# Performance work log

Hardware: AMD Instinct MI355X
Metric: run time of the kernel (lower is better)

Reference implementation:

```python
import jax, jax.numpy as jnp
import numpy as np

B, T, D_IN, D_H, D_OUT = 32, 2048, 1024, 1024, 1024

def setup_inputs() -> dict:
    key = jax.random.key(0)
    k1, k2, k3, k4, k5 = jax.random.split(key, 5)
    s = jax.random.normal(k1, (B, D_IN), dtype=jnp.float32)
    h = jax.random.normal(k2, (B, T, D_H), dtype=jnp.float32)
    # params (original uses np.random.random, i.e. uniform [0,1); scale kept modest)
    W_a = jax.random.uniform(k3, (D_IN, D_OUT), dtype=jnp.float32)
    U_a = jax.random.uniform(k4, (D_H, D_OUT), dtype=jnp.float32)
    v_a = jax.random.uniform(k5, (D_OUT,), dtype=jnp.float32)
    return {"s": s, "h": h, "W_a": W_a, "U_a": U_a, "v_a": v_a}

def reference(s, h, W_a, U_a, v_a):
    # Bahdanau additive attention:
    # e_bt = v_a . tanh(s W_a + h_t U_a);  a = softmax_t(e);  c_b = sum_t a_bt h_bt
    u_a_h = jnp.einsum('bth,ho->bto', h, U_a)            # [B,T,O]
    w_a_s = jnp.einsum('bi,io->bo', s, W_a)[:, None, :]  # [B,1,O]
    e = jnp.einsum('bto,o->bt', jnp.tanh(w_a_s + u_a_h), v_a)  # [B,T]
    a = jax.nn.softmax(e, axis=-1)                       # [B,T]
    c = jnp.einsum('bt,bth->bh', a, h)                   # [B,H]
    return c
```

## Files before the change

kernel.cpp:

```cpp
#include <hip/hip_runtime.h>
#include <hip/hip_bf16.h>
#include <stdint.h>

#define Bb 32
#define Tt 2048
#define Dd 1024

typedef float    f32x4 __attribute__((ext_vector_type(4)));
typedef _Float16 f16x8 __attribute__((ext_vector_type(8)));
typedef uint32_t u32;

#define WS_E     131072
#define WS_A     393216
#define WS_CP    655360
#define WS_UT    4849664

__device__ __forceinline__ void gll16(const void* g, const void* lds) {
  __builtin_amdgcn_global_load_lds(
      (const __attribute__((address_space(1))) u32*)(uintptr_t)g,
      (__attribute__((address_space(3))) u32*)(uint32_t)(uintptr_t)lds,
      16, 0, 0);
}

__global__ __launch_bounds__(256) void k_ws(const float* __restrict__ s,
                                            const float* __restrict__ W,
                                            float* __restrict__ w2_ws) {
  const int b = blockIdx.x >> 2;
  const int o = (blockIdx.x & 3) * 256 + threadIdx.x;
  __shared__ float s_sh[Dd];
#pragma unroll
  for (int j = 0; j < 4; ++j)
    s_sh[threadIdx.x + 256 * j] = s[b * Dd + threadIdx.x + 256 * j];
  __syncthreads();
  float acc = 0.f;
#pragma unroll 8
  for (int i = 0; i < Dd; ++i) acc += s_sh[i] * W[(size_t)i * Dd + o];
  w2_ws[b * Dd + o] = 2.f * acc;
}

__global__ __launch_bounds__(256) void k_ut(const float* __restrict__ U,
                                            uint8_t* __restrict__ U_ts) {
  const int i0 = (blockIdx.x >> 4) * 64;
  const int o0 = (blockIdx.x & 15) * 64;
  __shared__ float tile[64][65];
  const int tx = threadIdx.x & 63;
  const int ty = threadIdx.x >> 6;
#pragma unroll
  for (int jj = 0; jj < 16; ++jj)
    tile[tx][ty + 4 * jj] = U[(size_t)(i0 + ty + 4 * jj) * Dd + o0 + tx];
  __syncthreads();
#pragma unroll
  for (int it = 0; it < 2; ++it) {
    const int g = it * 256 + threadIdx.x;
    const int o_loc = g & 63;
    const int kg = g >> 6;
    const int o = o0 + o_loc;
    const int k = i0 + kg * 8;
    f16x8 r;
#pragma unroll
    for (int m = 0; m < 8; ++m) r[m] = (_Float16)tile[o_loc][kg * 8 + m];
    const int c    = (o >> 5) * 4 + (k >> 8);
    const int kk   = (k >> 5) & 7;
    const int half = (o >> 4) & 1;
    const int ln   = ((k >> 3) & 3) * 16 + (o & 15);
    *(f16x8*)(U_ts + (size_t)c * 16384 + kk * 2048 + half * 1024 + ln * 16) = r;
  }
}

__global__ __launch_bounds__(256, 2) void k_e(const float* __restrict__ h,
                                              const uint8_t* __restrict__ U_ts,
                                              const float* __restrict__ w2_ws,
                                              const float* __restrict__ v_a,
                                              float* __restrict__ e_ws) {
  const int b    = blockIdx.x >> 5;
  const int t0   = (blockIdx.x & 31) << 6;
  const int lane = threadIdx.x & 63;
  const int wv   = threadIdx.x >> 6;
  const int kh   = wv & 1;
  const int th   = wv >> 1;

  __shared__ __align__(16) uint8_t ubuf[3][16384];
  __shared__ __align__(16) float   exch[2048];
  __shared__ float w_sh[Dd];
  __shared__ float v_sh[Dd];

#pragma unroll
  for (int j = 0; j < 4; ++j) {
    const int o = threadIdx.x + 256 * j;
    w_sh[o] = w2_ws[b * Dd + o];
    v_sh[o] = v_a[o];
  }

  f16x8 hreg[32];
  {
    const int tcol = t0 + th * 32 + (lane & 15);
    const int kgrp = (lane >> 4) * 8;
    const float* hb0 = h + ((size_t)b * Tt + tcol) * Dd;
    const float* hb1 = hb0 + (size_t)16 * Dd;
#pragma unroll
    for (int ss = 0; ss < 16; ++ss) {
      const int kbase = (ss >> 2) * 256 + kh * 128 + (ss & 3) * 32 + kgrp;
      f32x4 p0 = *(const f32x4*)(hb0 + kbase);
      f32x4 p1 = *(const f32x4*)(hb0 + kbase + 4);
      f16x8 r;
      r[0] = (_Float16)p0[0]; r[1] = (_Float16)p0[1];
      r[2] = (_Float16)p0[2]; r[3] = (_Float16)p0[3];
      r[4] = (_Float16)p1[0]; r[5] = (_Float16)p1[1];
      r[6] = (_Float16)p1[2]; r[7] = (_Float16)p1[3];
      hreg[ss * 2] = r;
      p0 = *(const f32x4*)(hb1 + kbase);
      p1 = *(const f32x4*)(hb1 + kbase + 4);
      r[0] = (_Float16)p0[0]; r[1] = (_Float16)p0[1];
      r[2] = (_Float16)p0[2]; r[3] = (_Float16)p0[3];
      r[4] = (_Float16)p1[0]; r[5] = (_Float16)p1[1];
      r[6] = (_Float16)p1[2]; r[7] = (_Float16)p1[3];
      hreg[ss * 2 + 1] = r;
    }
  }

  asm volatile("s_waitcnt vmcnt(0) lgkmcnt(0)" ::: "memory");

  auto stage = [&](int c, int buf) {
    const uint8_t* src = U_ts + (size_t)c * 16384 + (size_t)(wv * 4) * 1024 + (size_t)lane * 16;
#pragma unroll
    for (int q = 0; q < 4; ++q)
      gll16(src + q * 1024, &ubuf[buf][(wv * 4 + q) * 1024]);
  };

  stage(0, 0);
  stage(1, 1);

  float ep0 = 0.f, ep1 = 0.f;
  const int obl = kh * 16 + ((lane >> 4) << 2);
  int cur = 0;

  for (int ot = 0; ot < 32; ++ot) {
    f32x4 accA0 = {0.f,0.f,0.f,0.f}, accA1 = {0.f,0.f,0.f,0.f};
    f32x4 accB0 = {0.f,0.f,0.f,0.f}, accB1 = {0.f,0.f,0.f,0.f};
#pragma unroll
    for (int kc = 0; kc < 4; ++kc) {
      const int c = ot * 4 + kc;
      asm volatile("s_waitcnt vmcnt(4)" ::: "memory");
      __builtin_amdgcn_sched_barrier(0);
      __builtin_amdgcn_s_barrier();
      __builtin_amdgcn_sched_barrier(0);
      const int nxt = cur >= 1 ? cur - 1 : cur + 2;
      stage((c + 2) & 127, nxt);
      const uint8_t* ub = &ubuf[cur][0] + kh * 8192 + lane * 16;
      __builtin_amdgcn_s_setprio(1);
#pragma unroll
      for (int kkl = 0; kkl < 4; ++kkl) {
        const f16x8 a0 = *(const f16x8*)(ub + kkl * 2048);
        const f16x8 a1 = *(const f16x8*)(ub + kkl * 2048 + 1024);
        const f16x8 b0 = hreg[(kc * 4 + kkl) * 2];
        const f16x8 b1 = hreg[(kc * 4 + kkl) * 2 + 1];
        accA0 = __builtin_amdgcn_mfma_f32_16x16x32_f16(a0, b0, accA0, 0, 0, 0);
        accA1 = __builtin_amdgcn_mfma_f32_16x16x32_f16(a0, b1, accA1, 0, 0, 0);
        accB0 = __builtin_amdgcn_mfma_f32_16x16x32_f16(a1, b0, accB0, 0, 0, 0);
        accB1 = __builtin_amdgcn_mfma_f32_16x16x32_f16(a1, b1, accB1, 0, 0, 0);
      }
      __builtin_amdgcn_s_setprio(0);
      cur = cur == 2 ? 0 : cur + 1;
    }
    {
      float* snd = exch + wv * 512 + lane * 4;
      if (kh == 0) { *(f32x4*)snd = accB0; *(f32x4*)(snd + 256) = accB1; }
      else         { *(f32x4*)snd = accA0; *(f32x4*)(snd + 256) = accA1; }
    }
    asm volatile("s_waitcnt lgkmcnt(0)" ::: "memory");
    __builtin_amdgcn_sched_barrier(0);
    __builtin_amdgcn_s_barrier();
    __builtin_amdgcn_sched_barrier(0);
    {
      const float* rcv = exch + (wv ^ 1) * 512 + lane * 4;
      const f32x4 q0 = *(const f32x4*)rcv;
      const f32x4 q1 = *(const f32x4*)(rcv + 256);
      f32x4 x0, x1;
      if (kh == 0) { x0 = accA0 + q0; x1 = accA1 + q1; }
      else         { x0 = accB0 + q0; x1 = accB1 + q1; }
      const int ob = (ot << 5) + obl;
#pragma unroll
      for (int r = 0; r < 4; ++r) {
        const float wr = w_sh[ob + r];
        const float vr = v_sh[ob + r];
        const float e0 = __expf(__builtin_fmaf(x0[r], 2.f, wr));
        const float e1 = __expf(__builtin_fmaf(x1[r], 2.f, wr));
        ep0 += vr * (1.f - 2.f / (e0 + 1.f));
        ep1 += vr * (1.f - 2.f / (e1 + 1.f));
      }
    }
  }

  ep0 += __shfl_xor(ep0, 16, 64); ep0 += __shfl_xor(ep0, 32, 64);
  ep1 += __shfl_xor(ep1, 16, 64); ep1 += __shfl_xor(ep1, 32, 64);
  __syncthreads();
  if (kh == 1 && lane < 16) {
    exch[th * 32 + lane]      = ep0;
    exch[th * 32 + 16 + lane] = ep1;
  }
  __syncthreads();
  if (kh == 0 && lane < 16) {
    e_ws[b * Tt + t0 + th * 32 + lane]      = ep0 + exch[th * 32 + lane];
    e_ws[b * Tt + t0 + th * 32 + 16 + lane] = ep1 + exch[th * 32 + 16 + lane];
  }
}

__global__ __launch_bounds__(256) void k_sm(const float* __restrict__ e_ws,
                                            float* __restrict__ a_ws) {
  const int b = blockIdx.x;
  const int lane = threadIdx.x & 63;
  const int wv = threadIdx.x >> 6;
  __shared__ float red[8];
  float ev[8];
  float m = -1e30f;
#pragma unroll
  for (int j = 0; j < 8; ++j) {
    ev[j] = e_ws[b * Tt + threadIdx.x + 256 * j];
    m = fmaxf(m, ev[j]);
  }
#pragma unroll
  for (int sft = 1; sft < 64; sft <<= 1) m = fmaxf(m, __shfl_xor(m, sft, 64));
  if (lane == 0) red[wv] = m;
  __syncthreads();
  m = fmaxf(fmaxf(red[0], red[1]), fmaxf(red[2], red[3]));
  float sum = 0.f;
#pragma unroll
  for (int j = 0; j < 8; ++j) { ev[j] = __expf(ev[j] - m); sum += ev[j]; }
#pragma unroll
  for (int sft = 1; sft < 64; sft <<= 1) sum += __shfl_xor(sum, sft, 64);
  if (lane == 0) red[4 + wv] = sum;
  __syncthreads();
  const float inv = 1.f / (red[4] + red[5] + red[6] + red[7]);
#pragma unroll
  for (int j = 0; j < 8; ++j) a_ws[b * Tt + threadIdx.x + 256 * j] = ev[j] * inv;
}

__global__ __launch_bounds__(256) void k_c1(const float* __restrict__ h,
                                            const float* __restrict__ a_ws,
                                            float* __restrict__ cpart) {
  const int b  = blockIdx.x >> 5;
  const int tc = blockIdx.x & 31;
  const int t0 = tc << 6;
  __shared__ float a_sh[64];
  if (threadIdx.x < 64) a_sh[threadIdx.x] = a_ws[b * Tt + t0 + threadIdx.x];
  __syncthreads();
  f32x4 acc = {0.f, 0.f, 0.f, 0.f};
  const float* hb = h + ((size_t)b * Tt + t0) * Dd + threadIdx.x * 4;
#pragma unroll 4
  for (int t = 0; t < 64; ++t) {
    const f32x4 hv = *(const f32x4*)(hb + (size_t)t * Dd);
    acc += a_sh[t] * hv;
  }
  *(f32x4*)(cpart + ((size_t)(tc * 32 + b) << 10) + threadIdx.x * 4) = acc;
}

__global__ __launch_bounds__(256) void k_c2(const float* __restrict__ cpart,
                                            float* __restrict__ out) {
  const int gid = blockIdx.x * 256 + threadIdx.x;
  const int b = gid >> 10;
  const int d = gid & 1023;
  float sv = 0.f;
#pragma unroll
  for (int tc = 0; tc < 32; ++tc) sv += cpart[((size_t)(tc * 32 + b) << 10) + d];
  out[gid] = sv;
}

extern "C" void kernel_launch(void* const* d_in, const int* in_sizes, int n_in,
                              void* d_out, int out_size, void* d_ws, size_t ws_size,
                              hipStream_t stream) {
  (void)in_sizes; (void)n_in; (void)out_size; (void)ws_size;
  const float* s  = (const float*)d_in[0];
  const float* h  = (const float*)d_in[1];
  const float* W  = (const float*)d_in[2];
  const float* U  = (const float*)d_in[3];
  const float* v  = (const float*)d_in[4];
  uint8_t* ws = (uint8_t*)d_ws;
  float*   w2_ws = (float*)ws;
  float*   e_ws  = (float*)(ws + WS_E);
  float*   a_ws  = (float*)(ws + WS_A);
  float*   cpart = (float*)(ws + WS_CP);
  uint8_t* U_ts  = ws + WS_UT;

  k_ws<<<128, 256, 0, stream>>>(s, W, w2_ws);
  k_ut<<<256, 256, 0, stream>>>(U, U_ts);
  k_e <<<1024, 256, 0, stream>>>(h, U_ts, w2_ws, v, e_ws);
  k_sm<<<Bb, 256, 0, stream>>>(e_ws, a_ws);
  k_c1<<<1024, 256, 0, stream>>>(h, a_ws, cpart);
  k_c2<<<128, 256, 0, stream>>>(cpart, (float*)d_out);
}
```

Before: 301.2 us.

## Split k_e reduction across 8 waves with two-stage cross-wave exchange

The scoring kernel now runs 512 threads per block. Each wave holds a quarter of the K dimension of h in registers (16 fragments instead of 32) and partial tiles are reduced across waves through two LDS exchange rounds. U staging drops from triple to double buffering with a full vmcnt(0) wait before each chunk. The aim is to cut VGPR pressure and raise occupancy and latency hiding. The cost is an extra barrier and exchange round per output tile and less prefetch depth.

Result: slower. 310.0 us (+2.9%).

```diff
diff --git a/kernel.cpp b/kernel.cpp
--- a/kernel.cpp
+++ b/kernel.cpp
@@ -67,142 +67,143 @@
   }
 }
 
-__global__ __launch_bounds__(256, 2) void k_e(const float* __restrict__ h,
+__global__ __launch_bounds__(512, 4) void k_e(const float* __restrict__ h,
                                               const uint8_t* __restrict__ U_ts,
                                               const float* __restrict__ w2_ws,
                                               const float* __restrict__ v_a,
                                               float* __restrict__ e_ws) {
   const int b    = blockIdx.x >> 5;
   const int t0   = (blockIdx.x & 31) << 6;
-  const int lane = threadIdx.x & 63;
-  const int wv   = threadIdx.x >> 6;
-  const int kh   = wv & 1;
-  const int th   = wv >> 1;
-
-  __shared__ __align__(16) uint8_t ubuf[3][16384];
-  __shared__ __align__(16) float   exch[2048];
+  const int tid  = threadIdx.x;
+  const int lane = tid & 63;
+  const int w    = tid >> 6;
+  const int th   = w >> 2;
+  const int kq   = w & 3;
+
+  __shared__ __align__(16) uint8_t ubuf[2][16384];
+  __shared__ __align__(16) float   exchA[4096];
+  __shared__ __align__(16) float   exchB[2048];
   __shared__ float w_sh[Dd];
   __shared__ float v_sh[Dd];
 
 #pragma unroll
-  for (int j = 0; j < 4; ++j) {
-    const int o = threadIdx.x + 256 * j;
+  for (int j = 0; j < 2; ++j) {
+    const int o = tid + 512 * j;
     w_sh[o] = w2_ws[b * Dd + o];
     v_sh[o] = v_a[o];
   }
 
-  f16x8 hreg[32];
+  f16x8 hreg[16];
   {
-    const int tcol = t0 + th * 32 + (lane & 15);
-    const int kgrp = (lane >> 4) * 8;
-    const float* hb0 = h + ((size_t)b * Tt + tcol) * Dd;
-    const float* hb1 = hb0 + (size_t)16 * Dd;
-#pragma unroll
-    for (int ss = 0; ss < 16; ++ss) {
-      const int kbase = (ss >> 2) * 256 + kh * 128 + (ss & 3) * 32 + kgrp;
-      f32x4 p0 = *(const f32x4*)(hb0 + kbase);
-      f32x4 p1 = *(const f32x4*)(hb0 + kbase + 4);
-      f16x8 r;
-      r[0] = (_Float16)p0[0]; r[1] = (_Float16)p0[1];
-      r[2] = (_Float16)p0[2]; r[3] = (_Float16)p0[3];
-      r[4] = (_Float16)p1[0]; r[5] = (_Float16)p1[1];
-      r[6] = (_Float16)p1[2]; r[7] = (_Float16)p1[3];
-      hreg[ss * 2] = r;
-      p0 = *(const f32x4*)(hb1 + kbase);
-      p1 = *(const f32x4*)(hb1 + kbase + 4);
-      r[0] = (_Float16)p0[0]; r[1] = (_Float16)p0[1];
-      r[2] = (_Float16)p0[2]; r[3] = (_Float16)p0[3];
-      r[4] = (_Float16)p1[0]; r[5] = (_Float16)p1[1];
-      r[6] = (_Float16)p1[2]; r[7] = (_Float16)p1[3];
-      hreg[ss * 2 + 1] = r;
-    }
-  }
-
-  asm volatile("s_waitcnt vmcnt(0) lgkmcnt(0)" ::: "memory");
+    const int lr = lane & 15, lg = (lane >> 4) * 8;
+#pragma unroll
+    for (int kc = 0; kc < 4; ++kc)
+#pragma unroll
+      for (int kkl = 0; kkl < 2; ++kkl)
+#pragma unroll
+        for (int tc = 0; tc < 2; ++tc) {
+          const int trow = t0 + th * 32 + tc * 16 + lr;
+          const int k = kc * 256 + kq * 64 + kkl * 32 + lg;
+          const float* p = h + ((size_t)b * Tt + trow) * Dd + k;
+          const f32x4 p0 = *(const f32x4*)p;
+          const f32x4 p1 = *(const f32x4*)(p + 4);
+          f16x8 r;
+          r[0] = (_Float16)p0[0]; r[1] = (_Float16)p0[1];
+          r[2] = (_Float16)p0[2]; r[3] = (_Float16)p0[3];
+          r[4] = (_Float16)p1[0]; r[5] = (_Float16)p1[1];
+          r[6] = (_Float16)p1[2]; r[7] = (_Float16)p1[3];
+          hreg[(kc * 2 + kkl) * 2 + tc] = r;
+        }
+  }
+  asm volatile("s_waitcnt lgkmcnt(0)" ::: "memory");
 
   auto stage = [&](int c, int buf) {
-    const uint8_t* src = U_ts + (size_t)c * 16384 + (size_t)(wv * 4) * 1024 + (size_t)lane * 16;
-#pragma unroll
-    for (int q = 0; q < 4; ++q)
-      gll16(src + q * 1024, &ubuf[buf][(wv * 4 + q) * 1024]);
+    const uint8_t* src = U_ts + (size_t)c * 16384 + (size_t)(2 * w) * 1024 + (size_t)lane * 16;
+    gll16(src,        &ubuf[buf][(2 * w) * 1024]);
+    gll16(src + 1024, &ubuf[buf][(2 * w + 1) * 1024]);
   };
 
   stage(0, 0);
-  stage(1, 1);
-
-  float ep0 = 0.f, ep1 = 0.f;
-  const int obl = kh * 16 + ((lane >> 4) << 2);
-  int cur = 0;
+
+  float ep = 0.f;
+  const int keepH = kq & 1;
+  const int keepT = (kq >> 1) & 1;
 
   for (int ot = 0; ot < 32; ++ot) {
-    f32x4 accA0 = {0.f,0.f,0.f,0.f}, accA1 = {0.f,0.f,0.f,0.f};
-    f32x4 accB0 = {0.f,0.f,0.f,0.f}, accB1 = {0.f,0.f,0.f,0.f};
+    f32x4 acc00 = {0.f,0.f,0.f,0.f};
+    f32x4 acc01 = {0.f,0.f,0.f,0.f};
+    f32x4 acc10 = {0.f,0.f,0.f,0.f};
+    f32x4 acc11 = {0.f,0.f,0.f,0.f};
 #pragma unroll
     for (int kc = 0; kc < 4; ++kc) {
       const int c = ot * 4 + kc;
-      asm volatile("s_waitcnt vmcnt(4)" ::: "memory");
+      asm volatile("s_waitcnt vmcnt(0)" ::: "memory");
       __builtin_amdgcn_sched_barrier(0);
       __builtin_amdgcn_s_barrier();
       __builtin_amdgcn_sched_barrier(0);
-      const int nxt = cur >= 1 ? cur - 1 : cur + 2;
-      stage((c + 2) & 127, nxt);
-      const uint8_t* ub = &ubuf[cur][0] + kh * 8192 + lane * 16;
+      const int cur = c & 1;
+      if (c + 1 < 128) stage(c + 1, cur ^ 1);
+      const uint8_t* ub = &ubuf[cur][(kq * 2) * 2048] + lane * 16;
       __builtin_amdgcn_s_setprio(1);
 #pragma unroll
-      for (int kkl = 0; kkl < 4; ++kkl) {
+      for (int kkl = 0; kkl < 2; ++kkl) {
         const f16x8 a0 = *(const f16x8*)(ub + kkl * 2048);
         const f16x8 a1 = *(const f16x8*)(ub + kkl * 2048 + 1024);
-        const f16x8 b0 = hreg[(kc * 4 + kkl) * 2];
-        const f16x8 b1 = hreg[(kc * 4 + kkl) * 2 + 1];
-        accA0 = __builtin_amdgcn_mfma_f32_16x16x32_f16(a0, b0, accA0, 0, 0, 0);
-        accA1 = __builtin_amdgcn_mfma_f32_16x16x32_f16(a0, b1, accA1, 0, 0, 0);
-        accB0 = __builtin_amdgcn_mfma_f32_16x16x32_f16(a1, b0, accB0, 0, 0, 0);
-        accB1 = __builtin_amdgcn_mfma_f32_16x16x32_f16(a1, b1, accB1, 0, 0, 0);
+        const f16x8 b0 = hreg[(kc * 2 + kkl) * 2];
+        const f16x8 b1 = hreg[(kc * 2 + kkl) * 2 + 1];
+        acc00 = __builtin_amdgcn_mfma_f32_16x16x32_f16(a0, b0, acc00, 0, 0, 0);
+        acc01 = __builtin_amdgcn_mfma_f32_16x16x32_f16(a0, b1, acc01, 0, 0, 0);
+        acc10 = __builtin_amdgcn_mfma_f32_16x16x32_f16(a1, b0, acc10, 0, 0, 0);
+        acc11 = __builtin_amdgcn_mfma_f32_16x16x32_f16(a1, b1, acc11, 0, 0, 0);
       }
       __builtin_amdgcn_s_setprio(0);
-      cur = cur == 2 ? 0 : cur + 1;
-    }
-    {
-      float* snd = exch + wv * 512 + lane * 4;
-      if (kh == 0) { *(f32x4*)snd = accB0; *(f32x4*)(snd + 256) = accB1; }
-      else         { *(f32x4*)snd = accA0; *(f32x4*)(snd + 256) = accA1; }
+    }
+    {
+      float* snd = exchA + w * 512 + lane * 4;
+      *(f32x4*)snd         = keepH ? acc00 : acc10;
+      *(f32x4*)(snd + 256) = keepH ? acc01 : acc11;
     }
     asm volatile("s_waitcnt lgkmcnt(0)" ::: "memory");
     __builtin_amdgcn_sched_barrier(0);
     __builtin_amdgcn_s_barrier();
     __builtin_amdgcn_sched_barrier(0);
-    {
-      const float* rcv = exch + (wv ^ 1) * 512 + lane * 4;
-      const f32x4 q0 = *(const f32x4*)rcv;
-      const f32x4 q1 = *(const f32x4*)(rcv + 256);
-      f32x4 x0, x1;
-      if (kh == 0) { x0 = accA0 + q0; x1 = accA1 + q1; }
-      else         { x0 = accB0 + q0; x1 = accB1 + q1; }
-      const int ob = (ot << 5) + obl;
-#pragma unroll
-      for (int r = 0; r < 4; ++r) {
-        const float wr = w_sh[ob + r];
-        const float vr = v_sh[ob + r];
-        const float e0 = __expf(__builtin_fmaf(x0[r], 2.f, wr));
-        const float e1 = __expf(__builtin_fmaf(x1[r], 2.f, wr));
-        ep0 += vr * (1.f - 2.f / (e0 + 1.f));
-        ep1 += vr * (1.f - 2.f / (e1 + 1.f));
-      }
-    }
-  }
-
-  ep0 += __shfl_xor(ep0, 16, 64); ep0 += __shfl_xor(ep0, 32, 64);
-  ep1 += __shfl_xor(ep1, 16, 64); ep1 += __shfl_xor(ep1, 32, 64);
-  __syncthreads();
-  if (kh == 1 && lane < 16) {
-    exch[th * 32 + lane]      = ep0;
-    exch[th * 32 + 16 + lane] = ep1;
-  }
-  __syncthreads();
-  if (kh == 0 && lane < 16) {
-    e_ws[b * Tt + t0 + th * 32 + lane]      = ep0 + exch[th * 32 + lane];
-    e_ws[b * Tt + t0 + th * 32 + 16 + lane] = ep1 + exch[th * 32 + 16 + lane];
-  }
+    f32x4 k0, k1;
+    {
+      const float* rcv = exchA + (w ^ 1) * 512 + lane * 4;
+      k0 = (keepH ? acc10 : acc00) + *(const f32x4*)rcv;
+      k1 = (keepH ? acc11 : acc01) + *(const f32x4*)(rcv + 256);
+    }
+    {
+      float* snd = exchB + w * 256 + lane * 4;
+      *(f32x4*)snd = keepT ? k0 : k1;
+    }
+    asm volatile("s_waitcnt lgkmcnt(0)" ::: "memory");
+    __builtin_amdgcn_sched_barrier(0);
+    __builtin_amdgcn_s_barrier();
+    __builtin_amdgcn_sched_barrier(0);
+    f32x4 xf;
+    {
+      const float* rcv = exchB + (w ^ 2) * 256 + lane * 4;
+      xf = (keepT ? k1 : k0) + *(const f32x4*)rcv;
+    }
+    const int ob = ot * 32 + keepH * 16 + ((lane >> 4) << 2);
+    const f32x4 w4 = *(const f32x4*)(w_sh + ob);
+    const f32x4 v4 = *(const f32x4*)(v_sh + ob);
+#pragma unroll
+    for (int r = 0; r < 4; ++r) {
+      const float e0 = __expf(__builtin_fmaf(xf[r], 2.f, w4[r]));
+      ep += v4[r] * (1.f - 2.f / (e0 + 1.f));
+    }
+  }
+
+  ep += __shfl_xor(ep, 16, 64);
+  ep += __shfl_xor(ep, 32, 64);
+  __syncthreads();
+  if ((kq & 1) && lane < 16) exchB[(th * 2 + keepT) * 16 + lane] = ep;
+  __syncthreads();
+  if (!(kq & 1) && lane < 16)
+    e_ws[b * Tt + t0 + th * 32 + keepT * 16 + lane] =
+        ep + exchB[(th * 2 + keepT) * 16 + lane];
 }
 
 __global__ __launch_bounds__(256) void k_sm(const float* __restrict__ e_ws,
@@ -283,7 +284,7 @@
 
   k_ws<<<128, 256, 0, stream>>>(s, W, w2_ws);
   k_ut<<<256, 256, 0, stream>>>(U, U_ts);
-  k_e <<<1024, 256, 0, stream>>>(h, U_ts, w2_ws, v, e_ws);
+  k_e <<<1024, 512, 0, stream>>>(h, U_ts, w2_ws, v, e_ws);
   k_sm<<<Bb, 256, 0, stream>>>(e_ws, a_ws);
   k_c1<<<1024, 256, 0, stream>>>(h, a_ws, cpart);
   k_c2<<<128, 256, 0, stream>>>(cpart, (float*)d_out);
```
